# Kernel optimization log

Measured on AMD Instinct MI355X. Metric: run time of the kernel, lower is better.

Reference implementation:

```python
import jax, jax.numpy as jnp
import numpy as np

MARGIN = 0.1
INF = 1e9  # matches self.inf in the torch module
NUM_OBJS = 256  # static upper bound on object ids (fill_max of pair_idx)


def setup_inputs() -> dict:
    key = jax.random.key(0)
    k1, k2 = jax.random.split(key)
    K, D = 8192, 768
    text_norm = jax.random.normal(k1, (K, D), dtype=jnp.float32)
    pair_idx = jax.random.randint(k2, (K, 2), 0, NUM_OBJS, dtype=jnp.int64)
    return {"text_norm": text_norm, "pair_idx": pair_idx}


def reference(text_norm, pair_idx):
    # text_norm: (K, D), pair_idx: (K, 2); grouping key is the object id pair_idx[:, 1].
    K = text_norm.shape[0]
    g = pair_idx[:, 1]

    # Full gram matrix of (normalized) text embeddings: (K, K)
    S = text_norm @ text_norm.T

    same = g[:, None] == g[None, :]          # same-object mask
    diag = jnp.eye(K, dtype=bool)

    # Per-row min over intra-group entries (diagonal excluded via +INF, as in torch eye*inf)
    row_min = jnp.min(jnp.where(same & ~diag, S, INF), axis=1)   # (K,)
    # Per-row max over cross-group entries
    row_max = jnp.max(jnp.where(~same, S, -INF), axis=1)          # (K,)

    # Reduce rows into per-object-group min/max (segment reductions over group id)
    gmin = jax.ops.segment_min(row_min, g, num_segments=NUM_OBJS)
    gmax = jax.ops.segment_max(row_max, g, num_segments=NUM_OBJS)
    counts = jax.ops.segment_sum(jnp.ones((K,), dtype=S.dtype), g, num_segments=NUM_OBJS)
    nonempty = counts > 0

    # max(0, -(score_min - score_max) + margin) per group, averaged over occupied groups
    per_group = jnp.maximum(0.0, gmax - gmin + MARGIN)
    loss = jnp.sum(jnp.where(nonempty, per_group, 0.0)) / jnp.sum(nonempty).astype(S.dtype)
    return loss
```

## Files before the change

kernel.cpp:

```cpp
#include <hip/hip_runtime.h>
#include <stdint.h>

#define KROWS 8192
#define DDIM  768
#define NUMG  256
#define BM    256
#define BN    128
#define BKB   128
#define NT    (DDIM / BKB)
#define TOTT  1056
#define MARGIN_F 0.1f
#define QSCALE (127.0f / 6.0f)
#define S2 ((6.0f / 127.0f) * (6.0f / 127.0f))

typedef int   i32x4 __attribute__((ext_vector_type(4)));
typedef long  i64x2 __attribute__((ext_vector_type(2)));

typedef __attribute__((address_space(3))) unsigned char lds_byte;
typedef __attribute__((address_space(1))) const unsigned char glob_byte;

__device__ __forceinline__ uint32_t enc_f32(float f) {
  uint32_t b = __float_as_uint(f);
  return (b & 0x80000000u) ? ~b : (b | 0x80000000u);
}
__device__ __forceinline__ float dec_f32(uint32_t u) {
  uint32_t b = (u & 0x80000000u) ? (u & 0x7FFFFFFFu) : ~u;
  return __uint_as_float(b);
}

__global__ void convert_k(const float* __restrict__ x, char* __restrict__ xb8,
                          const int* __restrict__ pidx, int* __restrict__ gids,
                          int* __restrict__ counts) {
  int t = blockIdx.x * blockDim.x + threadIdx.x;
  size_t e = 8 * (size_t)t;
  const float4* p = reinterpret_cast<const float4*>(x + e);
  float4 a = p[0], b = p[1];
  float v[8] = {a.x, a.y, a.z, a.w, b.x, b.y, b.z, b.w};
  unsigned long long u = 0;
#pragma unroll
  for (int j = 0; j < 8; ++j) {
    int q = (int)rintf(v[j] * QSCALE);
    q = q > 127 ? 127 : (q < -127 ? -127 : q);
    u |= ((unsigned long long)(unsigned char)(signed char)q) << (8 * j);
  }
  int row = (int)(e / DDIM);
  int k0  = (int)(e % DDIM);
  int g   = (k0 & 63) >> 3;
  size_t off = (size_t)row * DDIM + (k0 & ~63) + (g & 3) * 16 + (g >> 2) * 8;
  *reinterpret_cast<unsigned long long*>(xb8 + off) = u;
  if (t < KROWS) {
    int gg = pidx[2 * t + 1] & (NUMG - 1);
    gids[t] = gg;
    atomicAdd(&counts[gg], 1);
  }
}

__launch_bounds__(512, 4)
__global__ void gram_margin_k(const char* __restrict__ xb8,
                              const int* __restrict__ gids,
                              uint32_t* __restrict__ gmin,
                              uint32_t* __restrict__ gmax) {
  __shared__ char sA[BM * BKB];
  __shared__ char sB[BN * BKB];
  __shared__ uint32_t lgmin[NUMG];
  __shared__ uint32_t lgmax[NUMG];
  __shared__ int sgr[BM];
  __shared__ int sgc[BN];

  const int tid  = threadIdx.x;
  const int lane = tid & 63;
  const int wid  = tid >> 6;
  const int wr   = wid >> 1, wc = wid & 1;
  const int lr   = lane & 15, lh = lane >> 4;
  const int srow = tid >> 3;
  const int schunk = tid & 7;

  int phys = blockIdx.x;
  int idx  = (phys & 7) * (TOTT / 8) + (phys >> 3);
  int ib, jb;
  if (idx < 160) {
    int d = idx / 20, r = idx - d * 20;
    int i2 = (r < 2) ? 0 : (r < 6) ? 1 : (r < 12) ? 2 : 3;
    const int start[4] = {0, 2, 6, 12};
    int j2 = r - start[i2];
    ib = d * 4 + i2; jb = d * 8 + j2;
  } else {
    int e = idx - 160;
    int o = e >> 5, t = e & 31;
    int si = 1;
    while (si * (si + 1) / 2 <= o) ++si;
    int sj = o - si * (si - 1) / 2;
    ib = si * 4 + (t >> 3); jb = sj * 8 + (t & 7);
  }
  const int i0 = ib * BM, j0 = jb * BN;

  if (tid < NUMG) { lgmin[tid] = 0xFFFFFFFFu; lgmax[tid] = 0u; }
  if (tid < BM)   { sgr[tid] = gids[i0 + tid]; }
  if (tid < BN)   { sgc[tid] = gids[j0 + tid]; }

  i32x4 acc[4][4];
  const i32x4 zz = {0, 0, 0, 0};
#pragma unroll
  for (int m = 0; m < 4; ++m)
#pragma unroll
    for (int n = 0; n < 4; ++n) acc[m][n] = zz;

  for (int kt = 0; kt < NT; ++kt) {
    const int k0 = kt * BKB;
#pragma unroll
    for (int c = 0; c < 4; ++c) {
      int row = c * 64 + srow;
      int chunk = schunk ^ (row & 7);
      const char* ga = xb8 + (size_t)(i0 + row) * DDIM + k0 + chunk * 16;
      char* la = sA + (size_t)row * BKB + schunk * 16;
      __builtin_amdgcn_global_load_lds((glob_byte*)ga, (lds_byte*)la, 16, 0, 0);
    }
#pragma unroll
    for (int c = 0; c < 2; ++c) {
      int row = c * 64 + srow;
      int chunk = schunk ^ (row & 7);
      const char* gb = xb8 + (size_t)(j0 + row) * DDIM + k0 + chunk * 16;
      char* lb = sB + (size_t)row * BKB + schunk * 16;
      __builtin_amdgcn_global_load_lds((glob_byte*)gb, (lds_byte*)lb, 16, 0, 0);
    }
    __syncthreads();
#pragma unroll
    for (int ks2 = 0; ks2 < 2; ++ks2) {
      i64x2 av[4], bv[4];
#pragma unroll
      for (int m = 0; m < 4; ++m) {
        int row = wr * 64 + m * 16 + lr;
        int off = row * BKB + ((lh * 16 + ks2 * 64) ^ ((row & 7) << 4));
        av[m] = *reinterpret_cast<const i64x2*>(sA + off);
      }
#pragma unroll
      for (int n = 0; n < 4; ++n) {
        int row = wc * 64 + n * 16 + lr;
        int off = row * BKB + ((lh * 16 + ks2 * 64) ^ ((row & 7) << 4));
        bv[n] = *reinterpret_cast<const i64x2*>(sB + off);
      }
#pragma unroll
      for (int m = 0; m < 4; ++m)
#pragma unroll
        for (int n = 0; n < 4; ++n) {
          acc[m][n] = __builtin_amdgcn_mfma_i32_16x16x32_i8(av[m][0], bv[n][0],
                                                            acc[m][n], 0, 0, 0);
          acc[m][n] = __builtin_amdgcn_mfma_i32_16x16x32_i8(av[m][1], bv[n][1],
                                                            acc[m][n], 0, 0, 0);
        }
    }
    __syncthreads();
  }

  int gi[4][4];
#pragma unroll
  for (int m = 0; m < 4; ++m)
#pragma unroll
    for (int r = 0; r < 4; ++r) gi[m][r] = sgr[wr * 64 + m * 16 + lh * 4 + r];
  int gj[4];
#pragma unroll
  for (int n = 0; n < 4; ++n) gj[n] = sgc[wc * 64 + n * 16 + lr];

  float rmin[4][4], rmax[4][4], cmax[4];
#pragma unroll
  for (int m = 0; m < 4; ++m)
#pragma unroll
    for (int r = 0; r < 4; ++r) { rmin[m][r] = 3.0e38f; rmax[m][r] = -3.0e38f; }
#pragma unroll
  for (int n = 0; n < 4; ++n) cmax[n] = -3.0e38f;

  const bool offdiag = (i0 >= j0 + BN);
#pragma unroll
  for (int m = 0; m < 4; ++m) {
#pragma unroll
    for (int r = 0; r < 4; ++r) {
      int ii = i0 + wr * 64 + m * 16 + lh * 4 + r;
#pragma unroll
      for (int n = 0; n < 4; ++n) {
        int jj = j0 + wc * 64 + n * 16 + lr;
        float s = (float)acc[m][n][r] * S2;
        if (offdiag || (ii > jj)) {
          if (gi[m][r] == gj[n]) {
            rmin[m][r] = fminf(rmin[m][r], s);
          } else {
            rmax[m][r] = fmaxf(rmax[m][r], s);
            cmax[n] = fmaxf(cmax[n], s);
          }
        }
      }
    }
  }

#pragma unroll
  for (int s = 1; s <= 8; s <<= 1) {
#pragma unroll
    for (int m = 0; m < 4; ++m)
#pragma unroll
      for (int r = 0; r < 4; ++r) {
        rmin[m][r] = fminf(rmin[m][r], __shfl_xor(rmin[m][r], s, 64));
        rmax[m][r] = fmaxf(rmax[m][r], __shfl_xor(rmax[m][r], s, 64));
      }
  }
#pragma unroll
  for (int s = 16; s <= 32; s <<= 1)
#pragma unroll
    for (int n = 0; n < 4; ++n)
      cmax[n] = fmaxf(cmax[n], __shfl_xor(cmax[n], s, 64));

  if (lr == 0) {
#pragma unroll
    for (int m = 0; m < 4; ++m)
#pragma unroll
      for (int r = 0; r < 4; ++r) {
        if (rmin[m][r] < 1.0e38f) atomicMin(&lgmin[gi[m][r]], enc_f32(rmin[m][r]));
        if (rmax[m][r] > -1.0e38f) atomicMax(&lgmax[gi[m][r]], enc_f32(rmax[m][r]));
      }
  }
  if (lh == 0) {
#pragma unroll
    for (int n = 0; n < 4; ++n)
      if (cmax[n] > -1.0e38f) atomicMax(&lgmax[gj[n]], enc_f32(cmax[n]));
  }
  __syncthreads();

  if (tid < NUMG) {
    uint32_t mn = lgmin[tid], mx = lgmax[tid];
    if (mn != 0xFFFFFFFFu) atomicMin(&gmin[tid], mn);
    if (mx != 0u) atomicMax(&gmax[tid], mx);
  }
}

__global__ void finalize_k(const uint32_t* __restrict__ gmin,
                           const uint32_t* __restrict__ gmax,
                           const int* __restrict__ counts,
                           float* __restrict__ out) {
  __shared__ float s_num[256];
  __shared__ float s_den[256];
  int t = threadIdx.x;
  float per = 0.f, ne = 0.f;
  if (counts[t] > 0) {
    ne = 1.f;
    float mn = (gmin[t] == 0xFFFFFFFFu) ? 1.0e9f : dec_f32(gmin[t]);
    float mx = (gmax[t] == 0u) ? -1.0e9f : dec_f32(gmax[t]);
    per = fmaxf(0.0f, mx - mn + MARGIN_F);
  }
  s_num[t] = per;
  s_den[t] = ne;
  __syncthreads();
  for (int s = 128; s > 0; s >>= 1) {
    if (t < s) { s_num[t] += s_num[t + s]; s_den[t] += s_den[t + s]; }
    __syncthreads();
  }
  if (t == 0) out[0] = s_num[0] / s_den[0];
}

extern "C" void kernel_launch(void* const* d_in, const int* in_sizes, int n_in,
                              void* d_out, int out_size, void* d_ws, size_t ws_size,
                              hipStream_t stream) {
  const float* x   = (const float*)d_in[0];
  const int* pidx  = (const int*)d_in[1];
  float* out       = (float*)d_out;

  char* ws = (char*)d_ws;
  char* xb8 = ws;
  size_t off = (size_t)KROWS * DDIM;
  int* gids      = (int*)(ws + off); off += (size_t)KROWS * 4;
  uint32_t* gmin = (uint32_t*)(ws + off); off += NUMG * 4;
  uint32_t* gmax = (uint32_t*)(ws + off); off += NUMG * 4;
  int* counts    = (int*)(ws + off); off += NUMG * 4;

  hipMemsetAsync(gmin, 0xFF, NUMG * 4, stream);
  hipMemsetAsync(gmax, 0x00, NUMG * 8, stream);

  hipLaunchKernelGGL(convert_k, dim3((KROWS * DDIM / 8) / 256), dim3(256), 0, stream,
                     x, xb8, pidx, gids, counts);
  hipLaunchKernelGGL(gram_margin_k, dim3(TOTT), dim3(512), 0,
                     stream, xb8, gids, gmin, gmax);
  hipLaunchKernelGGL(finalize_k, dim3(1), dim3(NUMG), 0, stream,
                     gmin, gmax, counts, out);
}
```

Measured before the change: 88.13 us.

## Fuse finalize into gram kernel via ticket, drop memsets, use 16x16x64 int8 MFMA

Removes the two memset calls and the separate finalize kernel. Initialization of the group min/max buffers and a ticket counter moves into the convert kernel, and the last gram block to finish, detected with an atomic ticket, performs the final reduction. The inner product switches from pairs of 16x16x32 int8 MFMAs to a single 16x16x64 MFMA, which makes the store-side k permutation in convert unnecessary, so it becomes a plain linear store. Group occupancy is now inferred from a nonzero gmax instead of a separate counts array. That inference assumes every occupied group has some cross-group entry.

```diff
diff --git a/kernel.cpp b/kernel.cpp
--- a/kernel.cpp
+++ b/kernel.cpp
@@ -13,8 +13,7 @@
 #define QSCALE (127.0f / 6.0f)
 #define S2 ((6.0f / 127.0f) * (6.0f / 127.0f))
 
-typedef int   i32x4 __attribute__((ext_vector_type(4)));
-typedef long  i64x2 __attribute__((ext_vector_type(2)));
+typedef int i32x4 __attribute__((ext_vector_type(4)));
 
 typedef __attribute__((address_space(3))) unsigned char lds_byte;
 typedef __attribute__((address_space(1))) const unsigned char glob_byte;
@@ -30,7 +29,8 @@
 
 __global__ void convert_k(const float* __restrict__ x, char* __restrict__ xb8,
                           const int* __restrict__ pidx, int* __restrict__ gids,
-                          int* __restrict__ counts) {
+                          uint32_t* __restrict__ gmin, uint32_t* __restrict__ gmax,
+                          int* __restrict__ ticket) {
   int t = blockIdx.x * blockDim.x + threadIdx.x;
   size_t e = 8 * (size_t)t;
   const float4* p = reinterpret_cast<const float4*>(x + e);
@@ -43,15 +43,12 @@
     q = q > 127 ? 127 : (q < -127 ? -127 : q);
     u |= ((unsigned long long)(unsigned char)(signed char)q) << (8 * j);
   }
-  int row = (int)(e / DDIM);
-  int k0  = (int)(e % DDIM);
-  int g   = (k0 & 63) >> 3;
-  size_t off = (size_t)row * DDIM + (k0 & ~63) + (g & 3) * 16 + (g >> 2) * 8;
-  *reinterpret_cast<unsigned long long*>(xb8 + off) = u;
-  if (t < KROWS) {
-    int gg = pidx[2 * t + 1] & (NUMG - 1);
-    gids[t] = gg;
-    atomicAdd(&counts[gg], 1);
+  *reinterpret_cast<unsigned long long*>(xb8 + e) = u;
+  if (t < KROWS) gids[t] = pidx[2 * t + 1] & (NUMG - 1);
+  if (blockIdx.x == 0 && threadIdx.x < NUMG) {
+    gmin[threadIdx.x] = 0xFFFFFFFFu;
+    gmax[threadIdx.x] = 0u;
+    if (threadIdx.x == 0) *ticket = 0;
   }
 }
 
@@ -59,13 +56,16 @@
 __global__ void gram_margin_k(const char* __restrict__ xb8,
                               const int* __restrict__ gids,
                               uint32_t* __restrict__ gmin,
-                              uint32_t* __restrict__ gmax) {
+                              uint32_t* __restrict__ gmax,
+                              int* __restrict__ ticket,
+                              float* __restrict__ out) {
   __shared__ char sA[BM * BKB];
   __shared__ char sB[BN * BKB];
   __shared__ uint32_t lgmin[NUMG];
   __shared__ uint32_t lgmax[NUMG];
   __shared__ int sgr[BM];
   __shared__ int sgc[BN];
+  __shared__ int s_last;
 
   const int tid  = threadIdx.x;
   const int lane = tid & 63;
@@ -126,28 +126,25 @@
     __syncthreads();
 #pragma unroll
     for (int ks2 = 0; ks2 < 2; ++ks2) {
-      i64x2 av[4], bv[4];
+      i32x4 av[4], bv[4];
 #pragma unroll
       for (int m = 0; m < 4; ++m) {
         int row = wr * 64 + m * 16 + lr;
         int off = row * BKB + ((lh * 16 + ks2 * 64) ^ ((row & 7) << 4));
-        av[m] = *reinterpret_cast<const i64x2*>(sA + off);
+        av[m] = *reinterpret_cast<const i32x4*>(sA + off);
       }
 #pragma unroll
       for (int n = 0; n < 4; ++n) {
         int row = wc * 64 + n * 16 + lr;
         int off = row * BKB + ((lh * 16 + ks2 * 64) ^ ((row & 7) << 4));
-        bv[n] = *reinterpret_cast<const i64x2*>(sB + off);
+        bv[n] = *reinterpret_cast<const i32x4*>(sB + off);
       }
 #pragma unroll
       for (int m = 0; m < 4; ++m)
 #pragma unroll
-        for (int n = 0; n < 4; ++n) {
-          acc[m][n] = __builtin_amdgcn_mfma_i32_16x16x32_i8(av[m][0], bv[n][0],
+        for (int n = 0; n < 4; ++n)
+          acc[m][n] = __builtin_amdgcn_mfma_i32_16x16x64_i8(av[m], bv[n],
                                                             acc[m][n], 0, 0, 0);
-          acc[m][n] = __builtin_amdgcn_mfma_i32_16x16x32_i8(av[m][1], bv[n][1],
-                                                            acc[m][n], 0, 0, 0);
-        }
     }
     __syncthreads();
   }
@@ -228,30 +225,37 @@
     if (mn != 0xFFFFFFFFu) atomicMin(&gmin[tid], mn);
     if (mx != 0u) atomicMax(&gmax[tid], mx);
   }
-}
-
-__global__ void finalize_k(const uint32_t* __restrict__ gmin,
-                           const uint32_t* __restrict__ gmax,
-                           const int* __restrict__ counts,
-                           float* __restrict__ out) {
-  __shared__ float s_num[256];
-  __shared__ float s_den[256];
-  int t = threadIdx.x;
-  float per = 0.f, ne = 0.f;
-  if (counts[t] > 0) {
-    ne = 1.f;
-    float mn = (gmin[t] == 0xFFFFFFFFu) ? 1.0e9f : dec_f32(gmin[t]);
-    float mx = (gmax[t] == 0u) ? -1.0e9f : dec_f32(gmax[t]);
-    per = fmaxf(0.0f, mx - mn + MARGIN_F);
-  }
-  s_num[t] = per;
-  s_den[t] = ne;
   __syncthreads();
-  for (int s = 128; s > 0; s >>= 1) {
-    if (t < s) { s_num[t] += s_num[t + s]; s_den[t] += s_den[t + s]; }
+
+  if (tid == 0) {
+    __threadfence();
+    int fin = atomicAdd(ticket, 1);
+    s_last = (fin == TOTT - 1) ? 1 : 0;
+  }
+  __syncthreads();
+  if (s_last) {
+    __threadfence();
+    float* s_num = reinterpret_cast<float*>(lgmin);
+    float* s_den = reinterpret_cast<float*>(lgmax);
+    if (tid < NUMG) {
+      uint32_t mxbits = gmax[tid];
+      float per = 0.f, ne = 0.f;
+      if (mxbits != 0u) {
+        ne = 1.f;
+        float mn = (gmin[tid] == 0xFFFFFFFFu) ? 1.0e9f : dec_f32(gmin[tid]);
+        float mx = dec_f32(mxbits);
+        per = fmaxf(0.0f, mx - mn + MARGIN_F);
+      }
+      s_num[tid] = per;
+      s_den[tid] = ne;
+    }
     __syncthreads();
-  }
-  if (t == 0) out[0] = s_num[0] / s_den[0];
+    for (int s = 128; s > 0; s >>= 1) {
+      if (tid < s) { s_num[tid] += s_num[tid + s]; s_den[tid] += s_den[tid + s]; }
+      __syncthreads();
+    }
+    if (tid == 0) out[0] = s_num[0] / s_den[0];
+  }
 }
 
 extern "C" void kernel_launch(void* const* d_in, const int* in_sizes, int n_in,
@@ -267,15 +271,10 @@
   int* gids      = (int*)(ws + off); off += (size_t)KROWS * 4;
   uint32_t* gmin = (uint32_t*)(ws + off); off += NUMG * 4;
   uint32_t* gmax = (uint32_t*)(ws + off); off += NUMG * 4;
-  int* counts    = (int*)(ws + off); off += NUMG * 4;
-
-  hipMemsetAsync(gmin, 0xFF, NUMG * 4, stream);
-  hipMemsetAsync(gmax, 0x00, NUMG * 8, stream);
+  int* ticket    = (int*)(ws + off); off += 4;
 
   hipLaunchKernelGGL(convert_k, dim3((KROWS * DDIM / 8) / 256), dim3(256), 0, stream,
-                     x, xb8, pidx, gids, counts);
+                     x, xb8, pidx, gids, gmin, gmax, ticket);
   hipLaunchKernelGGL(gram_margin_k, dim3(TOTT), dim3(512), 0,
-                     stream, xb8, gids, gmin, gmax);
-  hipLaunchKernelGGL(finalize_k, dim3(1), dim3(NUMG), 0, stream,
-                     gmin, gmax, counts, out);
-}
+                     stream, xb8, gids, gmin, gmax, ticket, out);
+}
```

After: 86.03 us. 2.4% less time.
